# Optimization experiments

Measured on AMD Instinct MI355X. Metric: run time of the kernel, lower is better.

Reference implementation:

```python
import jax, jax.numpy as jnp
import numpy as np

N = 100000   # num_nodes
R = 200      # num_relations
DIM = 200    # hidden dim (in = out for every layer)
B = 30       # num_bases
L = 2        # num_layers
E = 800000   # num_edges


def setup_inputs() -> dict:
    key = jax.random.key(0)
    ks = jax.random.split(key, 7)
    edge_index = jax.random.randint(ks[0], (2, E), 0, N)
    edge_type = jax.random.randint(ks[1], (E,), 0, R)
    s = 1.0 / np.sqrt(DIM)
    emb = jax.random.normal(ks[2], (N, DIM), jnp.float32)
    comp = jax.random.normal(ks[3], (L, R, B), jnp.float32) * (1.0 / np.sqrt(B))
    bases = jax.random.normal(ks[4], (L, B, DIM, DIM), jnp.float32) * s
    root = jax.random.normal(ks[5], (L, DIM, DIM), jnp.float32) * s
    bias = jnp.zeros((L, DIM), jnp.float32)
    return dict(edge_index=edge_index, edge_type=edge_type, emb=emb,
                comp=comp, bases=bases, root=root, bias=bias)


def _rgcn_layer(x, src, dst, etype, comp_l, bases_l, root_l, bias_l):
    # Basis decomposition: W_r = sum_b comp[r, b] * bases[b]
    # msg_e = x[src_e] @ W_{etype_e}  computed as sum over bases (B is small & fixed)
    x_src = x[src]                      # [E, DIM] gather
    c = comp_l[etype]                   # [E, B] per-edge basis coefficients

    def body(acc, bc):
        basis_b, c_b = bc               # [DIM, DIM], [E]
        return acc + c_b[:, None] * (x_src @ basis_b), None

    acc0 = jnp.zeros((x_src.shape[0], root_l.shape[1]), x.dtype)
    msg, _ = jax.lax.scan(body, acc0, (bases_l, jnp.swapaxes(c, 0, 1)))  # [E, DIM]

    # PyG RGCNConv mean aggregation: normalize by in-degree per (dst node, relation)
    comb = dst * R + etype
    deg = jax.ops.segment_sum(jnp.ones((etype.shape[0],), x.dtype), comb,
                              num_segments=N * R)
    norm = 1.0 / jnp.maximum(deg[comb], 1.0)                             # [E]

    agg = jax.ops.segment_sum(msg * norm[:, None], dst, num_segments=N)  # [N, DIM]
    return agg + x @ root_l + bias_l


def reference(edge_index, edge_type, emb, comp, bases, root, bias):
    src, dst = edge_index[0], edge_index[1]
    x = emb
    for l in range(L):
        x = jax.nn.relu(_rgcn_layer(x, src, dst, edge_type,
                                    comp[l], bases[l], root[l], bias[l]))
        # dropout is identity in eval mode (deterministic reference)
    return x
```

## Files before the change

kernel.cpp:

```cpp
#include <hip/hip_runtime.h>
#include <hip/hip_bf16.h>
#include <stdint.h>

#define NN 100000
#define RR 200
#define DD 200
#define BB 30
#define LL 2
#define EE 800000

#define KP 224
#define NP 208
#define XP 224
#define AP 232
#define BPP 232
#define RT 128
#define MSGP 200
#define NSPL 2
#define MAXNC 24
#define NPART 128
#define EPB ((EE + NPART - 1) / NPART)

using bf16x8 = __attribute__((ext_vector_type(8))) short;
using f32x4  = __attribute__((ext_vector_type(4))) float;

#define OFF_NORM   0ull
#define OFF_SORT   3200000ull
#define OFF_CNT    6400000ull
#define OFF_XB     6404096ull
#define OFF_WT     51204096ull
#define OFF_ROOTT  69840896ull
#define OFF_CTL    69934080ull
#define OFF_POS    70065152ull
#define OFF_DSTCNT 73265152ull
#define OFF_DSTST  73665152ull
#define OFF_CUR    74065184ull
#define OFF_BLKH   74465184ull

static __device__ __forceinline__ short f2bf(float v) {
    union { __hip_bfloat16 h; short s; } u;
    u.h = __float2bfloat16(v);
    return u.s;
}

__global__ void kCount(const int* __restrict__ ei, const int* __restrict__ et,
                       unsigned int* __restrict__ deg8, int* __restrict__ dstCnt, int big) {
    int e = blockIdx.x * 256 + threadIdx.x;
    if (e >= EE) return;
    int d = ei[EE + e];
    int t = et[e];
    int comb = d * RR + t;
    atomicAdd(&deg8[comb >> 2], 1u << ((comb & 3) * 8));
    if (big) atomicAdd(&dstCnt[d], 1);
}

__global__ void kScanBlk(const int* __restrict__ dstCnt, int* __restrict__ dstStart,
                         int* __restrict__ blkSum) {
    __shared__ int s[256];
    int t = threadIdx.x, i = blockIdx.x * 256 + t;
    int v = (i < NN) ? dstCnt[i] : 0;
    s[t] = v;
    __syncthreads();
    #pragma unroll
    for (int off = 1; off < 256; off <<= 1) {
        int x = (t >= off) ? s[t - off] : 0;
        __syncthreads();
        s[t] += x;
        __syncthreads();
    }
    if (i < NN) dstStart[i] = s[t] - v;
    if (t == 255) blkSum[blockIdx.x] = s[255];
}
__global__ void kScanTop(int* __restrict__ blkSum, int nblk) {
    __shared__ int s[512];
    int t = threadIdx.x;
    int v = (t < nblk) ? blkSum[t] : 0;
    s[t] = v;
    __syncthreads();
    #pragma unroll
    for (int off = 1; off < 512; off <<= 1) {
        int x = (t >= off) ? s[t - off] : 0;
        __syncthreads();
        s[t] += x;
        __syncthreads();
    }
    if (t < nblk) blkSum[t] = s[t] - v;
}
__global__ void kScanAdd(const int* __restrict__ dstCnt, int* __restrict__ dstStart,
                         const int* __restrict__ blkSum) {
    int i = blockIdx.x * 256 + threadIdx.x;
    if (i >= NN) return;
    int v = dstStart[i] + blkSum[blockIdx.x];
    dstStart[i] = v;
    if (i == NN - 1) dstStart[NN] = v + dstCnt[i];
}

__global__ void kChunk(const int* __restrict__ dstStart, int* __restrict__ bS,
                       int* __restrict__ cesS, int NC, int T) {
    int tid = threadIdx.x;
    if (tid > NC) return;
    int v;
    if (tid == NC) v = NN;
    else if (tid == 0) v = 0;
    else {
        int target = tid * T;
        int lo = 0, hi = NN;
        while (lo < hi) {
            int mid = (lo + hi) >> 1;
            if (dstStart[mid] >= target) hi = mid; else lo = mid + 1;
        }
        v = lo;
    }
    bS[tid] = v;
    cesS[tid] = dstStart[v];
}

__global__ __launch_bounds__(256) void kHist(const int* __restrict__ ei,
        const int* __restrict__ et, const int* __restrict__ bS,
        int* __restrict__ blockHist, int NC) {
    __shared__ int hist[MAXNC * RR];
    __shared__ int bsh[MAXNC + 1];
    int tid = threadIdx.x, b = blockIdx.x;
    int NB = NC * RR;
    if (tid <= NC) bsh[tid] = bS[tid];
    for (int i = tid; i < NB; i += 256) hist[i] = 0;
    __syncthreads();
    int ebeg = b * EPB, eend = min(EE, ebeg + EPB);
    for (int e = ebeg + tid; e < eend; e += 256) {
        int d = ei[EE + e];
        int t = et[e];
        int c = 0;
        for (int j = 1; j < NC; ++j) if (d >= bsh[j]) c = j;
        atomicAdd(&hist[c * RR + t], 1);
    }
    __syncthreads();
    for (int i = tid; i < NB; i += 256)
        blockHist[(size_t)b * NB + i] = hist[i];
}

__global__ __launch_bounds__(128) void kScanP(int* __restrict__ blockHist,
                                              int* __restrict__ cntB, int NB) {
    __shared__ int s[NPART];
    int t = threadIdx.x, k = blockIdx.x;
    int v = blockHist[(size_t)t * NB + k];
    s[t] = v;
    __syncthreads();
    #pragma unroll
    for (int off = 1; off < NPART; off <<= 1) {
        int x = (t >= off) ? s[t - off] : 0;
        __syncthreads();
        s[t] += x;
        __syncthreads();
    }
    blockHist[(size_t)t * NB + k] = s[t] - v;
    if (t == NPART - 1) cntB[k] = s[NPART - 1];
}

__global__ void kScanB(const int* __restrict__ cntB, int* __restrict__ relStartB,
                       int* __restrict__ cursorB, int nb) {
    __shared__ int c[MAXNC * RR];
    __shared__ int rs[MAXNC * RR + 1];
    int tid = threadIdx.x;
    for (int i = tid; i < nb; i += 256) c[i] = cntB[i];
    __syncthreads();
    if (tid == 0) {
        int s = 0;
        for (int i = 0; i < nb; ++i) {
            rs[i] = s;
            s += c[i];
        }
        rs[nb] = s;
    }
    __syncthreads();
    for (int i = tid; i <= nb; i += 256) {
        relStartB[i] = rs[i];
        if (i < nb) cursorB[i] = rs[i];
    }
}

__global__ __launch_bounds__(256) void kPart(const int* __restrict__ ei,
        const int* __restrict__ et, const unsigned int* __restrict__ deg8,
        const int* __restrict__ bS, const int* __restrict__ relStartB,
        const int* __restrict__ blockHist, const int* __restrict__ dstStart,
        int* __restrict__ cur, float* __restrict__ norm, int* __restrict__ sortedE,
        int* __restrict__ posDst, int NC) {
    __shared__ int curL[MAXNC * RR];
    __shared__ int bsh[MAXNC + 1];
    int tid = threadIdx.x, b = blockIdx.x;
    int NB = NC * RR;
    if (tid <= NC) bsh[tid] = bS[tid];
    for (int i = tid; i < NB; i += 256)
        curL[i] = relStartB[i] + blockHist[(size_t)b * NB + i];
    __syncthreads();
    int ebeg = b * EPB, eend = min(EE, ebeg + EPB);
    for (int e = ebeg + tid; e < eend; e += 256) {
        int d = ei[EE + e];
        int t = et[e];
        int comb = d * RR + t;
        unsigned int deg = (deg8[comb >> 2] >> ((comb & 3) * 8)) & 0xffu;
        norm[e] = 1.0f / (float)(deg ? deg : 1u);
        int c = 0;
        for (int j = 1; j < NC; ++j) if (d >= bsh[j]) c = j;
        int pos = atomicAdd(&curL[c * RR + t], 1);
        sortedE[pos] = e;
        posDst[e] = dstStart[d] + atomicAdd(&cur[d], 1);
    }
}

__global__ void kCountB(const int* __restrict__ ei, const int* __restrict__ et,
                        const int* __restrict__ bS, int* __restrict__ cntB, int NC) {
    __shared__ int bsh[MAXNC + 1];
    if (threadIdx.x <= NC) bsh[threadIdx.x] = bS[threadIdx.x];
    __syncthreads();
    int e = blockIdx.x * 256 + threadIdx.x;
    if (e >= EE) return;
    int d = ei[EE + e];
    int t = et[e];
    int c = 0;
    for (int j = 1; j < NC; ++j) if (d >= bsh[j]) c = j;
    atomicAdd(&cntB[c * RR + t], 1);
}

__global__ void kNormScatter(const int* __restrict__ ei, const int* __restrict__ et,
                             const unsigned int* __restrict__ deg8, const int* __restrict__ bS,
                             int* __restrict__ cursorB, const int* __restrict__ dstStart,
                             int* __restrict__ cur, float* __restrict__ norm,
                             int* __restrict__ sortedE, int* __restrict__ posDst,
                             int NC, int big) {
    __shared__ int bsh[MAXNC + 1];
    if (threadIdx.x <= NC) bsh[threadIdx.x] = bS[threadIdx.x];
    __syncthreads();
    int e = blockIdx.x * 256 + threadIdx.x;
    if (e >= EE) return;
    int d = ei[EE + e];
    int t = et[e];
    int comb = d * RR + t;
    unsigned int deg = (deg8[comb >> 2] >> ((comb & 3) * 8)) & 0xffu;
    norm[e] = 1.0f / (float)(deg ? deg : 1u);
    int c = 0;
    for (int j = 1; j < NC; ++j) if (d >= bsh[j]) c = j;
    int pos = atomicAdd(&cursorB[c * RR + t], 1);
    sortedE[pos] = e;
    if (big) posDst[e] = dstStart[d] + atomicAdd(&cur[d], 1);
}

__global__ void kConvert(const float* __restrict__ x, short* __restrict__ xb, int doRelu) {
    int idx = blockIdx.x * 256 + threadIdx.x;
    if (idx >= NN * XP) return;
    int i = idx / XP, col = idx - i * XP;
    float v = 0.0f;
    if (col < DD) {
        v = x[i * DD + col];
        if (doRelu) v = fmaxf(v, 0.0f);
    }
    xb[idx] = (col < DD) ? f2bf(v) : (short)0;
}

__global__ void kRelu(float* __restrict__ y) {
    int idx = blockIdx.x * 256 + threadIdx.x;
    if (idx < NN * DD) y[idx] = fmaxf(y[idx], 0.0f);
}

__global__ __launch_bounds__(256) void kW(const float* __restrict__ comp,
                                          const float* __restrict__ bases,
                                          short* __restrict__ Wt) {
    int kt = blockIdx.x;
    int ng = blockIdx.y;
    int tid = threadIdx.x;
    int k = kt * 32 + (tid & 31);
    int n = ng * 8 + (tid >> 5);
    bool live = (k < DD) && (n < DD);
    float vb[BB];
    #pragma unroll
    for (int b = 0; b < BB; ++b)
        vb[b] = live ? bases[((size_t)b * DD + k) * DD + n] : 0.0f;
    size_t wo = (size_t)n * KP + k;
    for (int r = 0; r < RR; ++r) {
        float a = 0.0f;
        #pragma unroll
        for (int b = 0; b < BB; ++b) a += comp[r * BB + b] * vb[b];
        Wt[(size_t)r * (NP * KP) + wo] = f2bf(a);
    }
}

__global__ void kRootT(const float* __restrict__ root, short* __restrict__ rootT) {
    int idx = blockIdx.x * 256 + threadIdx.x;
    if (idx >= NP * KP) return;
    int n = idx / KP, k = idx - n * KP;
    rootT[idx] = (n < DD && k < DD) ? f2bf(root[k * DD + n]) : (short)0;
}

template<int F0, int NF>
__device__ __forceinline__ void gemmHalf2(const short* As, const short* bCol,
                                          int arow0, int arow1, int kg,
                                          f32x4* acc0, f32x4* acc1) {
    #pragma unroll
    for (int f = 0; f < NF; ++f) {
        acc0[f] = (f32x4){0.f, 0.f, 0.f, 0.f};
        acc1[f] = (f32x4){0.f, 0.f, 0.f, 0.f};
    }
    bf16x8 bb[2][NF];
    #pragma unroll
    for (int f = 0; f < NF; ++f)
        bb[0][f] = *(const bf16x8*)(bCol + (size_t)(F0 + f) * 16 * KP);
    #pragma unroll
    for (int kc = 0; kc < 7; ++kc) {
        if (kc < 6) {
            #pragma unroll
            for (int f = 0; f < NF; ++f)
                bb[(kc + 1) & 1][f] = *(const bf16x8*)(bCol + (size_t)(F0 + f) * 16 * KP + (kc + 1) * 32);
        }
        bf16x8 a0 = *(const bf16x8*)(&As[arow0 * AP + kc * 32 + kg]);
        bf16x8 a1 = *(const bf16x8*)(&As[arow1 * AP + kc * 32 + kg]);
        #pragma unroll
        for (int f = 0; f < NF; ++f) {
            acc0[f] = __builtin_amdgcn_mfma_f32_16x16x32_bf16(a0, bb[kc & 1][f], acc0[f], 0, 0, 0);
            acc1[f] = __builtin_amdgcn_mfma_f32_16x16x32_bf16(a1, bb[kc & 1][f], acc1[f], 0, 0, 0);
        }
    }
}

__global__ __launch_bounds__(256) void kRootGemm(const short* __restrict__ xb,
        const short* __restrict__ rootT, const float* __restrict__ bias,
        float* __restrict__ y) {
    __shared__ short As[RT * AP];
    int i0 = blockIdx.x * RT;
    int tid = threadIdx.x;
    int rowL = tid >> 1, sub = tid & 1;
    int i = i0 + rowL;
    for (int c = sub; c < 28; c += 2) {
        int4 v = make_int4(0, 0, 0, 0);
        if (i < NN) v = *(const int4*)(xb + (size_t)i * XP + c * 8);
        *(int4*)(&As[rowL * AP + c * 8]) = v;
    }
    __syncthreads();
    int lane = tid & 63, wave = tid >> 6;
    int arow0 = wave * 32 + (lane & 15);
    int arow1 = arow0 + 16;
    int kg = (lane >> 4) * 8;
    const short* bCol = rootT + (lane & 15) * KP + kg;
    int colLane = lane & 15;
    int rbase = i0 + wave * 32 + (lane >> 4) * 4;
    {
        f32x4 acc0[7], acc1[7];
        gemmHalf2<0, 7>(As, bCol, arow0, arow1, kg, acc0, acc1);
        #pragma unroll
        for (int f = 0; f < 7; ++f) {
            int col = f * 16 + colLane;
            float bv = bias[col];
            #pragma unroll
            for (int j = 0; j < 4; ++j) {
                int r0 = rbase + j, r1 = rbase + 16 + j;
                if (r0 < NN) y[(size_t)r0 * DD + col] = acc0[f][j] + bv;
                if (r1 < NN) y[(size_t)r1 * DD + col] = acc1[f][j] + bv;
            }
        }
    }
    {
        f32x4 acc0[6], acc1[6];
        gemmHalf2<7, 6>(As, bCol, arow0, arow1, kg, acc0, acc1);
        #pragma unroll
        for (int f = 0; f < 6; ++f) {
            int col = (7 + f) * 16 + colLane;
            if (col < DD) {
                float bv = bias[col];
                #pragma unroll
                for (int j = 0; j < 4; ++j) {
                    int r0 = rbase + j, r1 = rbase + 16 + j;
                    if (r0 < NN) y[(size_t)r0 * DD + col] = acc0[f][j] + bv;
                    if (r1 < NN) y[(size_t)r1 * DD + col] = acc1[f][j] + bv;
                }
            }
        }
    }
}

template<int MODE>
__global__ __launch_bounds__(512) void kMsgP(const int* __restrict__ ei,
        const short* __restrict__ xb, const short* __restrict__ Wt,
        const int* __restrict__ relStartB, const int* __restrict__ sortedE,
        const float* __restrict__ norm, const int* __restrict__ posDst,
        const int* __restrict__ cesS, float* __restrict__ y,
        short* __restrict__ msg, int c) {
    __shared__ short Bp[NP * BPP];
    int r = blockIdx.x / NSPL;
    int h = blockIdx.x - r * NSPL;
    int relStart = relStartB[c * RR + r];
    int eEnd     = relStartB[c * RR + r + 1];
    int nE = eEnd - relStart;
    if (nE <= 0) return;
    int tid = threadIdx.x;
    {
        const short* wp = Wt + (size_t)r * (NP * KP);
        for (int idx = tid; idx < NP * (KP / 8); idx += 512) {
            int n = idx / (KP / 8);
            int k8 = idx - n * (KP / 8);
            int4 v = *(const int4*)(wp + (size_t)n * KP + k8 * 8);
            *(int4*)(&Bp[n * BPP + k8 * 8]) = v;
        }
    }
    __syncthreads();
    int lane = tid & 63, wave = tid >> 6;
    int colLane = lane & 15;
    int kg = (lane >> 4) * 8;
    int rbase = (lane >> 4) * 4;
    int nwt = (nE + 15) / 16;
    int ces = (MODE == 0) ? cesS[c] : 0;

    bf16x8 aC[7], aN[7];
    int psC[4], psN[4];
    float nmC[4], nmN[4];

    auto loadTile = [&](int wt, bf16x8* a, int* ps, float* nm) {
        int eBase = relStart + wt * 16;
        int eIdxA = eBase + colLane;
        int eidA = sortedE[min(eIdxA, eEnd - 1)];
        int srcA = ei[eidA];
        const short* aRow = xb + (size_t)srcA * XP;
        #pragma unroll
        for (int kc = 0; kc < 7; ++kc)
            a[kc] = *(const bf16x8*)(aRow + kc * 32 + kg);
        #pragma unroll
        for (int j = 0; j < 4; ++j) {
            int eI = eBase + rbase + j;
            bool v = eI < eEnd;
            int eid = v ? sortedE[eI] : 0;
            nm[j] = v ? norm[eid] : 0.0f;
            if (MODE == 0) ps[j] = v ? (posDst[eid] - ces) : -1;
            else           ps[j] = v ? ei[EE + eid] : -1;
        }
    };

    int wt = h * 8 + wave;
    if (wt < nwt) loadTile(wt, aC, psC, nmC);
    for (; wt < nwt; wt += NSPL * 8) {
        int wtn = wt + NSPL * 8;
        if (wtn < nwt) loadTile(wtn, aN, psN, nmN);
        f32x4 acc[13];
        #pragma unroll
        for (int f = 0; f < 13; ++f) acc[f] = (f32x4){0.f, 0.f, 0.f, 0.f};
        #pragma unroll
        for (int kc = 0; kc < 7; ++kc) {
            bf16x8 bb[13];
            #pragma unroll
            for (int f = 0; f < 13; ++f)
                bb[f] = *(const bf16x8*)(&Bp[(f * 16 + colLane) * BPP + kc * 32 + kg]);
            #pragma unroll
            for (int f = 0; f < 13; ++f)
                acc[f] = __builtin_amdgcn_mfma_f32_16x16x32_bf16(aC[kc], bb[f], acc[f], 0, 0, 0);
        }
        #pragma unroll
        for (int j = 0; j < 4; ++j) {
            int ps = psC[j]; float nm = nmC[j];
            if (ps >= 0) {
                #pragma unroll
                for (int f = 0; f < 13; ++f) {
                    int col = f * 16 + colLane;
                    if (col < DD) {
                        float val = acc[f][j] * nm;
                        if (MODE == 0) msg[(size_t)ps * MSGP + col] = f2bf(val);
                        else           atomicAdd(&y[(size_t)ps * DD + col], val);
                    }
                }
            }
        }
        if (wtn < nwt) {
            #pragma unroll
            for (int kc = 0; kc < 7; ++kc) aC[kc] = aN[kc];
            #pragma unroll
            for (int j = 0; j < 4; ++j) { psC[j] = psN[j]; nmC[j] = nmN[j]; }
        }
    }
}

__global__ __launch_bounds__(256) void kAgg(const short* __restrict__ msg,
        const int* __restrict__ dstStart, const int* __restrict__ bS,
        const int* __restrict__ cesS, float* __restrict__ y, int c) {
    int wv = threadIdx.x >> 6, lane = threadIdx.x & 63;
    int b0 = bS[c], b1 = bS[c + 1];
    int ces = cesS[c];
    int gw = blockIdx.x * 4 + wv;
    int nw = gridDim.x * 4;
    for (int d = b0 + gw; d < b1; d += nw) {
        int s = dstStart[d] - ces, e = dstStart[d + 1] - ces;
        float a0 = 0.f, a1 = 0.f, a2 = 0.f, a3 = 0.f;
        if (lane < 50) {
            for (int j = s; j < e; ++j) {
                int2 v = *(const int2*)(msg + (size_t)j * MSGP + lane * 4);
                unsigned u0 = (unsigned)v.x, u1 = (unsigned)v.y;
                a0 += __uint_as_float(u0 << 16);
                a1 += __uint_as_float(u0 & 0xffff0000u);
                a2 += __uint_as_float(u1 << 16);
                a3 += __uint_as_float(u1 & 0xffff0000u);
            }
            int colBase = lane * 4;
            float4 rv = *(const float4*)(y + (size_t)d * DD + colBase);
            float4 o;
            o.x = fmaxf(rv.x + a0, 0.f);
            o.y = fmaxf(rv.y + a1, 0.f);
            o.z = fmaxf(rv.z + a2, 0.f);
            o.w = fmaxf(rv.w + a3, 0.f);
            *(float4*)(y + (size_t)d * DD + colBase) = o;
        }
    }
}

extern "C" void kernel_launch(void* const* d_in, const int* in_sizes, int n_in,
                              void* d_out, int out_size, void* d_ws, size_t ws_size,
                              hipStream_t stream) {
    (void)in_sizes; (void)n_in; (void)out_size;
    const int*   ei    = (const int*)d_in[0];
    const int*   et    = (const int*)d_in[1];
    const float* emb   = (const float*)d_in[2];
    const float* comp  = (const float*)d_in[3];
    const float* bases = (const float*)d_in[4];
    const float* root  = (const float*)d_in[5];
    const float* bias  = (const float*)d_in[6];
    float* y = (float*)d_out;
    char* ws = (char*)d_ws;
    float* norm    = (float*)(ws + OFF_NORM);
    int*   sortedE = (int*)(ws + OFF_SORT);
    short* xb      = (short*)(ws + OFF_XB);
    short* Wt      = (short*)(ws + OFF_WT);
    short* rootT   = (short*)(ws + OFF_ROOTT);
    int*   posDst  = (int*)(ws + OFF_POS);
    int*   dstCnt  = (int*)(ws + OFF_DSTCNT);
    int*   dstStart= (int*)(ws + OFF_DSTST);
    int*   cur     = (int*)(ws + OFF_CUR);
    int*   blockHist = (int*)(ws + OFF_BLKH);
    unsigned int* deg8 = (unsigned int*)(ws + OFF_XB);

    int NC = 0;
    long long T = EE;
    unsigned long long msgOff = 0;
    for (int cc = 1; cc <= MAXNC; ++cc) {
        long long t = (EE + cc - 1) / cc;
        unsigned long long mo = OFF_BLKH + (unsigned long long)NPART * cc * RR * 4;
        unsigned long long need = mo + (unsigned long long)(t + 64) * (MSGP * 2);
        if ((unsigned long long)ws_size >= need) { NC = cc; T = t; msgOff = mo; break; }
    }
    int big = (NC > 0) ? 1 : 0;
    if (!big) { NC = 1; T = EE; msgOff = OFF_BLKH; }
    short* msg = (short*)(ws + msgOff);

    int *cntB, *relStartB, *cursorB, *bS, *cesS, *blkSum;
    if (big) {
        int* ctl = (int*)(ws + OFF_CTL);
        cntB = ctl; relStartB = ctl + 4864; cursorB = ctl + 9728;
        bS = ctl + 19456; cesS = ctl + 19520; blkSum = ctl + 19584;
    } else {
        int* ctl = (int*)(ws + OFF_CNT);
        cntB = ctl; relStartB = ctl + 256; cursorB = ctl + 512;
        bS = ctl + 976; cesS = ctl + 992; blkSum = ctl + 1000;
    }

    const int NBLK = (NN + 255) / 256;

    hipMemsetAsync(deg8, 0, (size_t)NN * RR, stream);
    if (big) {
        hipMemsetAsync(dstCnt, 0, (size_t)NN * 4, stream);
        hipMemsetAsync(cur, 0, (size_t)NN * 4, stream);
    } else {
        hipMemsetAsync((void*)cntB, 0, 4096, stream);
    }

    kCount<<<(EE + 255) / 256, 256, 0, stream>>>(ei, et, deg8, dstCnt, big);
    if (big) {
        kScanBlk<<<NBLK, 256, 0, stream>>>(dstCnt, dstStart, blkSum);
        kScanTop<<<1, 512, 0, stream>>>(blkSum, NBLK);
        kScanAdd<<<NBLK, 256, 0, stream>>>(dstCnt, dstStart, blkSum);
        kChunk<<<1, 64, 0, stream>>>(dstStart, bS, cesS, NC, (int)T);
        kHist<<<NPART, 256, 0, stream>>>(ei, et, bS, blockHist, NC);
        kScanP<<<NC * RR, NPART, 0, stream>>>(blockHist, cntB, NC * RR);
        kScanB<<<1, 256, 0, stream>>>(cntB, relStartB, cursorB, NC * RR);
        kPart<<<NPART, 256, 0, stream>>>(ei, et, deg8, bS, relStartB, blockHist,
                                         dstStart, cur, norm, sortedE, posDst, NC);
    } else {
        kCountB<<<(EE + 255) / 256, 256, 0, stream>>>(ei, et, bS, cntB, NC);
        kScanB<<<1, 256, 0, stream>>>(cntB, relStartB, cursorB, NC * RR);
        kNormScatter<<<(EE + 255) / 256, 256, 0, stream>>>(ei, et, deg8, bS, cursorB,
                                                           dstStart, cur, norm, sortedE,
                                                           posDst, NC, big);
    }
    kConvert<<<(NN * XP + 255) / 256, 256, 0, stream>>>(emb, xb, 0);

    for (int l = 0; l < LL; ++l) {
        kW<<<dim3(7, 26), 256, 0, stream>>>(comp + l * RR * BB,
                                            bases + (size_t)l * BB * DD * DD, Wt);
        kRootT<<<(NP * KP + 255) / 256, 256, 0, stream>>>(root + l * DD * DD, rootT);
        kRootGemm<<<(NN + RT - 1) / RT, 256, 0, stream>>>(xb, rootT, bias + l * DD, y);
        if (big) {
            for (int c = 0; c < NC; ++c) {
                kMsgP<0><<<RR * NSPL, 512, 0, stream>>>(ei, xb, Wt, relStartB, sortedE,
                                                        norm, posDst, cesS, y, msg, c);
                kAgg<<<2048, 256, 0, stream>>>(msg, dstStart, bS, cesS, y, c);
            }
            if (l == 0)
                kConvert<<<(NN * XP + 255) / 256, 256, 0, stream>>>(y, xb, 0);
        } else {
            kMsgP<1><<<RR * NSPL, 512, 0, stream>>>(ei, xb, Wt, relStartB, sortedE,
                                                    norm, posDst, cesS, y, msg, 0);
            if (l == 0) kConvert<<<(NN * XP + 255) / 256, 256, 0, stream>>>(y, xb, 1);
            else        kRelu<<<(NN * DD + 255) / 256, 256, 0, stream>>>(y);
        }
    }
}
```

Baseline: 1.294 ms.

## Process 32-edge tiles per wave to reuse LDS weight fragments across two row blocks

Each wave now handles two 16-edge row blocks per tile instead of one. The output columns are split into two passes of 7 and 6 column fragments, so each LDS-loaded B fragment feeds two MFMAs. This halves LDS weight reads per edge and keeps the accumulator register count bounded. In exchange it doubles the prefetched A registers and per-tile edge work, which may raise register pressure and lower occupancy, and coarser tiles can waste more work on relations with few edges.

```diff
diff --git a/kernel.cpp b/kernel.cpp
--- a/kernel.cpp
+++ b/kernel.cpp
@@ -404,30 +404,33 @@
     int colLane = lane & 15;
     int kg = (lane >> 4) * 8;
     int rbase = (lane >> 4) * 4;
-    int nwt = (nE + 15) / 16;
+    int nwt = (nE + 31) / 32;
     int ces = (MODE == 0) ? cesS[c] : 0;
 
-    bf16x8 aC[7], aN[7];
-    int psC[4], psN[4];
-    float nmC[4], nmN[4];
-
-    auto loadTile = [&](int wt, bf16x8* a, int* ps, float* nm) {
-        int eBase = relStart + wt * 16;
-        int eIdxA = eBase + colLane;
-        int eidA = sortedE[min(eIdxA, eEnd - 1)];
-        int srcA = ei[eidA];
-        const short* aRow = xb + (size_t)srcA * XP;
+    bf16x8 aC[2][7], aN[2][7];
+    int psC[2][4], psN[2][4];
+    float nmC[2][4], nmN[2][4];
+
+    auto loadTile = [&](int wt, bf16x8 (*a)[7], int (*ps)[4], float (*nm)[4]) {
+        int eBase = relStart + wt * 32;
         #pragma unroll
-        for (int kc = 0; kc < 7; ++kc)
-            a[kc] = *(const bf16x8*)(aRow + kc * 32 + kg);
-        #pragma unroll
-        for (int j = 0; j < 4; ++j) {
-            int eI = eBase + rbase + j;
-            bool v = eI < eEnd;
-            int eid = v ? sortedE[eI] : 0;
-            nm[j] = v ? norm[eid] : 0.0f;
-            if (MODE == 0) ps[j] = v ? (posDst[eid] - ces) : -1;
-            else           ps[j] = v ? ei[EE + eid] : -1;
+        for (int m = 0; m < 2; ++m) {
+            int eIdxA = eBase + m * 16 + colLane;
+            int eidA = sortedE[min(eIdxA, eEnd - 1)];
+            int srcA = ei[eidA];
+            const short* aRow = xb + (size_t)srcA * XP;
+            #pragma unroll
+            for (int kc = 0; kc < 7; ++kc)
+                a[m][kc] = *(const bf16x8*)(aRow + kc * 32 + kg);
+            #pragma unroll
+            for (int j = 0; j < 4; ++j) {
+                int eI = eBase + m * 16 + rbase + j;
+                bool v = eI < eEnd;
+                int eid = v ? sortedE[eI] : 0;
+                nm[m][j] = v ? norm[eid] : 0.0f;
+                if (MODE == 0) ps[m][j] = v ? (posDst[eid] - ces) : -1;
+                else           ps[m][j] = v ? ei[EE + eid] : -1;
+            }
         }
     };
 
@@ -436,39 +439,88 @@
     for (; wt < nwt; wt += NSPL * 8) {
         int wtn = wt + NSPL * 8;
         if (wtn < nwt) loadTile(wtn, aN, psN, nmN);
-        f32x4 acc[13];
-        #pragma unroll
-        for (int f = 0; f < 13; ++f) acc[f] = (f32x4){0.f, 0.f, 0.f, 0.f};
-        #pragma unroll
-        for (int kc = 0; kc < 7; ++kc) {
-            bf16x8 bb[13];
-            #pragma unroll
-            for (int f = 0; f < 13; ++f)
-                bb[f] = *(const bf16x8*)(&Bp[(f * 16 + colLane) * BPP + kc * 32 + kg]);
-            #pragma unroll
-            for (int f = 0; f < 13; ++f)
-                acc[f] = __builtin_amdgcn_mfma_f32_16x16x32_bf16(aC[kc], bb[f], acc[f], 0, 0, 0);
-        }
-        #pragma unroll
-        for (int j = 0; j < 4; ++j) {
-            int ps = psC[j]; float nm = nmC[j];
-            if (ps >= 0) {
-                #pragma unroll
-                for (int f = 0; f < 13; ++f) {
-                    int col = f * 16 + colLane;
-                    if (col < DD) {
-                        float val = acc[f][j] * nm;
-                        if (MODE == 0) msg[(size_t)ps * MSGP + col] = f2bf(val);
-                        else           atomicAdd(&y[(size_t)ps * DD + col], val);
+        {
+            f32x4 acc0[7], acc1[7];
+            #pragma unroll
+            for (int f = 0; f < 7; ++f) {
+                acc0[f] = (f32x4){0.f, 0.f, 0.f, 0.f};
+                acc1[f] = (f32x4){0.f, 0.f, 0.f, 0.f};
+            }
+            #pragma unroll
+            for (int kc = 0; kc < 7; ++kc) {
+                bf16x8 bb[7];
+                #pragma unroll
+                for (int f = 0; f < 7; ++f)
+                    bb[f] = *(const bf16x8*)(&Bp[(f * 16 + colLane) * BPP + kc * 32 + kg]);
+                #pragma unroll
+                for (int f = 0; f < 7; ++f) {
+                    acc0[f] = __builtin_amdgcn_mfma_f32_16x16x32_bf16(aC[0][kc], bb[f], acc0[f], 0, 0, 0);
+                    acc1[f] = __builtin_amdgcn_mfma_f32_16x16x32_bf16(aC[1][kc], bb[f], acc1[f], 0, 0, 0);
+                }
+            }
+            #pragma unroll
+            for (int m = 0; m < 2; ++m) {
+                #pragma unroll
+                for (int j = 0; j < 4; ++j) {
+                    int ps = psC[m][j]; float nm = nmC[m][j];
+                    if (ps >= 0) {
+                        #pragma unroll
+                        for (int f = 0; f < 7; ++f) {
+                            int col = f * 16 + colLane;
+                            float val = (m ? acc1[f][j] : acc0[f][j]) * nm;
+                            if (MODE == 0) msg[(size_t)ps * MSGP + col] = f2bf(val);
+                            else           atomicAdd(&y[(size_t)ps * DD + col], val);
+                        }
                     }
                 }
             }
         }
+        {
+            f32x4 acc0[6], acc1[6];
+            #pragma unroll
+            for (int f = 0; f < 6; ++f) {
+                acc0[f] = (f32x4){0.f, 0.f, 0.f, 0.f};
+                acc1[f] = (f32x4){0.f, 0.f, 0.f, 0.f};
+            }
+            #pragma unroll
+            for (int kc = 0; kc < 7; ++kc) {
+                bf16x8 bb[6];
+                #pragma unroll
+                for (int f = 0; f < 6; ++f)
+                    bb[f] = *(const bf16x8*)(&Bp[((7 + f) * 16 + colLane) * BPP + kc * 32 + kg]);
+                #pragma unroll
+                for (int f = 0; f < 6; ++f) {
+                    acc0[f] = __builtin_amdgcn_mfma_f32_16x16x32_bf16(aC[0][kc], bb[f], acc0[f], 0, 0, 0);
+                    acc1[f] = __builtin_amdgcn_mfma_f32_16x16x32_bf16(aC[1][kc], bb[f], acc1[f], 0, 0, 0);
+                }
+            }
+            #pragma unroll
+            for (int m = 0; m < 2; ++m) {
+                #pragma unroll
+                for (int j = 0; j < 4; ++j) {
+                    int ps = psC[m][j]; float nm = nmC[m][j];
+                    if (ps >= 0) {
+                        #pragma unroll
+                        for (int f = 0; f < 6; ++f) {
+                            int col = (7 + f) * 16 + colLane;
+                            if (col < DD) {
+                                float val = (m ? acc1[f][j] : acc0[f][j]) * nm;
+                                if (MODE == 0) msg[(size_t)ps * MSGP + col] = f2bf(val);
+                                else           atomicAdd(&y[(size_t)ps * DD + col], val);
+                            }
+                        }
+                    }
+                }
+            }
+        }
         if (wtn < nwt) {
             #pragma unroll
-            for (int kc = 0; kc < 7; ++kc) aC[kc] = aN[kc];
-            #pragma unroll
-            for (int j = 0; j < 4; ++j) { psC[j] = psN[j]; nmC[j] = nmN[j]; }
+            for (int m = 0; m < 2; ++m) {
+                #pragma unroll
+                for (int kc = 0; kc < 7; ++kc) aC[m][kc] = aN[m][kc];
+                #pragma unroll
+                for (int j = 0; j < 4; ++j) { psC[m][j] = psN[m][j]; nmC[m][j] = nmN[m][j]; }
+            }
         }
     }
 }
```

After: 1.263 ms. 1.02x faster.
